# Kernel tuning notes

Hardware: AMD Instinct MI355X
Metric: run time of the kernel (lower is better)

Reference implementation:

```python
import jax, jax.numpy as jnp
import numpy as np

N_NODES = 50000
EPS = 1e-12  # F.normalize eps


def _gcn_layer(x, W, b, src, dst):
    # GCNConv(normalize=False): h = x @ W, then sum-aggregate messages from
    # source nodes into target nodes along edge_index, then add bias.
    h = x @ W
    agg = jax.ops.segment_sum(h[src], dst, num_segments=N_NODES)
    out = agg + b
    # F.normalize(p=2, dim=-1) then ReLU
    norm = jnp.linalg.norm(out, axis=-1, keepdims=True)
    out = out / jnp.maximum(norm, EPS)
    return jax.nn.relu(out)


def setup_inputs() -> dict:
    key = jax.random.key(0)
    ks = jax.random.split(key, 8)
    nfeat, nhid, nclass, n_edges = 128, 128, 40, 640000
    x = jax.random.normal(ks[0], (N_NODES, nfeat), dtype=jnp.float32)
    edge_index = jax.random.randint(ks[1], (2, n_edges), 0, N_NODES, dtype=jnp.int64)
    s = 1.0 / np.sqrt(nhid)
    return {
        "x": x,
        "edge_index": edge_index,
        "W1": jax.random.normal(ks[2], (nfeat, nhid), jnp.float32) * s,
        "b1": jnp.zeros((nhid,), jnp.float32),
        "W2": jax.random.normal(ks[3], (nhid, nhid), jnp.float32) * s,
        "b2": jnp.zeros((nhid,), jnp.float32),
        "W3": jax.random.normal(ks[4], (nhid, nhid), jnp.float32) * s,
        "b3": jnp.zeros((nhid,), jnp.float32),
        "W4": jax.random.normal(ks[5], (nhid, nhid), jnp.float32) * s,
        "b4": jnp.zeros((nhid,), jnp.float32),
        "Wl": jax.random.normal(ks[6], (nhid, nclass), jnp.float32) * s,
        "bl": jnp.zeros((nclass,), jnp.float32),
    }


def reference(x, edge_index, W1, b1, W2, b2, W3, b3, W4, b4, Wl, bl):
    src, dst = edge_index[0], edge_index[1]
    x1 = _gcn_layer(x, W1, b1, src, dst)
    x2 = _gcn_layer(x1, W2, b2, src, dst)
    x3 = _gcn_layer(x2, W3, b3, src, dst)
    x4 = _gcn_layer(x3, W4, b4, src, dst)
    logits = x4 @ Wl + bl
    probs = jax.nn.softmax(logits, axis=-1)
    return (logits, probs, x4)
```

## Files before the change

kernel.cpp:

```cpp
#include <hip/hip_runtime.h>
#include <hip/hip_bf16.h>
#include <hip/hip_fp16.h>
#include <math.h>

#define NFEAT 128
#define NCLASS 40

typedef __attribute__((ext_vector_type(8))) short frag_ab;
typedef __attribute__((ext_vector_type(4))) float frag_cd;

static __device__ inline unsigned short f2bf_rne(float f) {
    union { float f; unsigned u; } v;
    v.f = f;
    unsigned r = v.u + 0x7FFFu + ((v.u >> 16) & 1u);
    return (unsigned short)(r >> 16);
}
static __device__ inline float bf2f(unsigned short h) {
    union { unsigned u; float f; } v;
    v.u = ((unsigned)h) << 16;
    return v.f;
}


__global__ __launch_bounds__(256) void prep_kernel(const float* __restrict__ x,
                                                   __half* __restrict__ xh, int xc4,
                                                   int* __restrict__ cnt, int n_nodes,
                                                   const float* __restrict__ W0,
                                                   const float* __restrict__ W1,
                                                   const float* __restrict__ W2,
                                                   const float* __restrict__ W3,
                                                   short* __restrict__ whi,
                                                   short* __restrict__ wlo,
                                                   int convB, int zeroB) {
    int b = blockIdx.x;
    if (b < convB) {
        int i = b * 256 + threadIdx.x;
        if (i < xc4) {
            float4 v = ((const float4*)x)[i];
            ((__half2*)xh)[i * 2 + 0] = __floats2half2_rn(v.x, v.y);
            ((__half2*)xh)[i * 2 + 1] = __floats2half2_rn(v.z, v.w);
        }
    } else if (b < convB + zeroB) {
        int i = (b - convB) * 256 + threadIdx.x;
        if (i < n_nodes) cnt[i] = 0;
    } else {
        int wb = b - convB - zeroB;
        int layer = wb >> 3;
        const float* W = layer == 0 ? W0 : layer == 1 ? W1 : layer == 2 ? W2 : W3;
        short* h = whi + (size_t)layer * 16384;
        short* l = wlo + (size_t)layer * 16384;
        int idx = (wb & 7) * 256 + threadIdx.x;
        int lane = idx & 63;
        int t = (idx >> 6) & 7;
        int s = idx >> 9;
        int quad = lane >> 4;
        int n = lane & 15;
        int kbase = s * 32 + quad * 8;
        int col = t * 16 + n;
#pragma unroll
        for (int j = 0; j < 8; ++j) {
            float f = W[(size_t)(kbase + j) * NFEAT + col];
            unsigned short hb = f2bf_rne(f);
            unsigned short lb = f2bf_rne(f - bf2f(hb));
            h[(size_t)idx * 8 + j] = (short)hb;
            l[(size_t)idx * 8 + j] = (short)lb;
        }
    }
}


__global__ __launch_bounds__(256) void hist_kernel(const int* __restrict__ dst,
                                                   int* __restrict__ counts, int n_edges) {
    int i = blockIdx.x * 256 + threadIdx.x;
    int n4 = n_edges >> 2;
    if (i < n4) {
        int4 d = ((const int4*)dst)[i];
        atomicAdd(&counts[d.x], 1);
        atomicAdd(&counts[d.y], 1);
        atomicAdd(&counts[d.z], 1);
        atomicAdd(&counts[d.w], 1);
    }
    if (i == 0) {
        for (int e = n4 << 2; e < n_edges; ++e) atomicAdd(&counts[dst[e]], 1);
    }
}

__global__ __launch_bounds__(256) void scan1_kernel(const int* __restrict__ cnt,
                                                    int* __restrict__ excl,
                                                    int* __restrict__ bsums, int n) {
    __shared__ int sd[256];
    int t = threadIdx.x;
    int i = blockIdx.x * 256 + t;
    int v = (i < n) ? cnt[i] : 0;
    sd[t] = v;
    __syncthreads();
#pragma unroll
    for (int off = 1; off < 256; off <<= 1) {
        int tmp = (t >= off) ? sd[t - off] : 0;
        __syncthreads();
        sd[t] += tmp;
        __syncthreads();
    }
    if (i < n) excl[i] = sd[t] - v;
    if (t == 255) bsums[blockIdx.x] = sd[255];
}

__global__ __launch_bounds__(256) void scan2_kernel(int* __restrict__ bsums, int nb) {
    __shared__ int sd[256];
    int t = threadIdx.x;
    int v = (t < nb) ? bsums[t] : 0;
    sd[t] = v;
    __syncthreads();
#pragma unroll
    for (int off = 1; off < 256; off <<= 1) {
        int tmp = (t >= off) ? sd[t - off] : 0;
        __syncthreads();
        sd[t] += tmp;
        __syncthreads();
    }
    if (t < nb) bsums[t] = sd[t] - v;
    if (t == 255) bsums[nb] = sd[255];
}

__global__ __launch_bounds__(256) void scan3_kernel(const int* __restrict__ excl,
                                                    const int* __restrict__ bsums,
                                                    int* __restrict__ row_ptr,
                                                    int* __restrict__ woff, int n, int nb) {
    int i = blockIdx.x * 256 + threadIdx.x;
    if (i < n) {
        int v = excl[i] + bsums[blockIdx.x];
        row_ptr[i] = v;
        woff[i] = v;
    }
    if (i == 0) row_ptr[n] = bsums[nb];
}

__global__ __launch_bounds__(256) void scatter_kernel(const int* __restrict__ src,
                                                      const int* __restrict__ dst,
                                                      int* __restrict__ woff,
                                                      int* __restrict__ src_sorted, int n_edges) {
    int i = blockIdx.x * 256 + threadIdx.x;
    int n4 = n_edges >> 2;
    if (i < n4) {
        int4 d = ((const int4*)dst)[i];
        int4 s = ((const int4*)src)[i];
        int p0 = atomicAdd(&woff[d.x], 1);
        int p1 = atomicAdd(&woff[d.y], 1);
        int p2 = atomicAdd(&woff[d.z], 1);
        int p3 = atomicAdd(&woff[d.w], 1);
        src_sorted[p0] = s.x;
        src_sorted[p1] = s.y;
        src_sorted[p2] = s.z;
        src_sorted[p3] = s.w;
    }
    if (i == 0) {
        for (int e = n4 << 2; e < n_edges; ++e) {
            int p = atomicAdd(&woff[dst[e]], 1);
            src_sorted[p] = src[e];
        }
    }
}


__global__ __launch_bounds__(256) void agg_h_kernel(const __half* __restrict__ xin,
                                                    const int* __restrict__ row_ptr,
                                                    const int* __restrict__ src_sorted,
                                                    __half* __restrict__ aggh, int n_nodes) {
    int node = blockIdx.x * 16 + (threadIdx.x >> 4);
    if (node >= n_nodes) return;
    int c = threadIdx.x & 15;
    int jb = row_ptr[node], je = row_ptr[node + 1];
    const uint4* xp = (const uint4*)xin;

    float a[8];
#pragma unroll
    for (int i = 0; i < 8; ++i) a[i] = 0.f;

    int j = jb;
    for (; j + 3 < je; j += 4) {
        int s0 = src_sorted[j];
        int s1 = src_sorted[j + 1];
        int s2 = src_sorted[j + 2];
        int s3 = src_sorted[j + 3];
        uint4 r0 = xp[s0 * 16 + c];
        uint4 r1 = xp[s1 * 16 + c];
        uint4 r2 = xp[s2 * 16 + c];
        uint4 r3 = xp[s3 * 16 + c];
#pragma unroll
        for (int q = 0; q < 4; ++q) {
            unsigned u0 = (&r0.x)[q], u1 = (&r1.x)[q], u2 = (&r2.x)[q], u3 = (&r3.x)[q];
            float2 f0 = __half22float2(*(__half2*)&u0);
            float2 f1 = __half22float2(*(__half2*)&u1);
            float2 f2 = __half22float2(*(__half2*)&u2);
            float2 f3 = __half22float2(*(__half2*)&u3);
            a[q * 2 + 0] += f0.x + f1.x + f2.x + f3.x;
            a[q * 2 + 1] += f0.y + f1.y + f2.y + f3.y;
        }
    }
    for (; j < je; ++j) {
        int s0 = src_sorted[j];
        uint4 r0 = xp[s0 * 16 + c];
#pragma unroll
        for (int q = 0; q < 4; ++q) {
            unsigned u0 = (&r0.x)[q];
            float2 f0 = __half22float2(*(__half2*)&u0);
            a[q * 2 + 0] += f0.x;
            a[q * 2 + 1] += f0.y;
        }
    }
    __half2 h0 = __floats2half2_rn(a[0], a[1]);
    __half2 h1 = __floats2half2_rn(a[2], a[3]);
    __half2 h2 = __floats2half2_rn(a[4], a[5]);
    __half2 h3 = __floats2half2_rn(a[6], a[7]);
    uint4 o;
    o.x = *(unsigned*)&h0; o.y = *(unsigned*)&h1; o.z = *(unsigned*)&h2; o.w = *(unsigned*)&h3;
    ((uint4*)aggh)[(size_t)node * 16 + c] = o;
}


__global__ __launch_bounds__(256) void gemm_mfma_kernel(const __half* __restrict__ A,
                                                        const short* __restrict__ whi,
                                                        const short* __restrict__ wlo,
                                                        const float* __restrict__ bias,
                                                        float* __restrict__ outf,
                                                        __half* __restrict__ outh, int M) {
    int tid = threadIdx.x;
    int wave = tid >> 6;
    int lane = tid & 63;
    int quad = lane >> 4;
    int n16 = lane & 15;
    int base = blockIdx.x * 64;

    int arow = base + wave * 16 + n16;
    int arc = arow < M ? arow : M - 1;
    const __half* Ar = A + (size_t)arc * NFEAT;

    const frag_ab* WH = (const frag_ab*)whi;
    const frag_ab* WL = (const frag_ab*)wlo;

    frag_cd acc[8];
#pragma unroll
    for (int t = 0; t < 8; ++t) acc[t] = (frag_cd){0.f, 0.f, 0.f, 0.f};

#pragma unroll
    for (int s = 0; s < 4; ++s) {
        uint4 av = *(const uint4*)(Ar + s * 32 + quad * 8);
        frag_ab ah, al;
#pragma unroll
        for (int q = 0; q < 4; ++q) {
            unsigned u = (&av.x)[q];
            float2 f = __half22float2(*(__half2*)&u);
            unsigned short hb0 = f2bf_rne(f.x);
            unsigned short hb1 = f2bf_rne(f.y);
            ah[q * 2 + 0] = (short)hb0;
            ah[q * 2 + 1] = (short)hb1;
            al[q * 2 + 0] = (short)f2bf_rne(f.x - bf2f(hb0));
            al[q * 2 + 1] = (short)f2bf_rne(f.y - bf2f(hb1));
        }
#pragma unroll
        for (int t = 0; t < 8; ++t) {
            frag_ab bh = WH[(s * 8 + t) * 64 + lane];
            frag_ab bl = WL[(s * 8 + t) * 64 + lane];
            acc[t] = __builtin_amdgcn_mfma_f32_16x16x32_bf16(ah, bh, acc[t], 0, 0, 0);
            acc[t] = __builtin_amdgcn_mfma_f32_16x16x32_bf16(ah, bl, acc[t], 0, 0, 0);
            acc[t] = __builtin_amdgcn_mfma_f32_16x16x32_bf16(al, bh, acc[t], 0, 0, 0);
        }
    }

    float ssq[4] = {0.f, 0.f, 0.f, 0.f};
#pragma unroll
    for (int t = 0; t < 8; ++t) {
        float bv = bias[t * 16 + n16];
#pragma unroll
        for (int r = 0; r < 4; ++r) {
            acc[t][r] += bv;
            ssq[r] += acc[t][r] * acc[t][r];
        }
    }
#pragma unroll
    for (int mask = 1; mask <= 8; mask <<= 1) {
#pragma unroll
        for (int r = 0; r < 4; ++r) ssq[r] += __shfl_xor(ssq[r], mask);
    }
    float inv[4];
#pragma unroll
    for (int r = 0; r < 4; ++r) inv[r] = 1.0f / fmaxf(sqrtf(ssq[r]), 1e-12f);

    int orow0 = base + wave * 16 + quad * 4;
#pragma unroll
    for (int r = 0; r < 4; ++r) {
        int orow = orow0 + r;
        if (orow < M) {
            if (outh) {
                __half* op = outh + (size_t)orow * NFEAT + n16;
#pragma unroll
                for (int t = 0; t < 8; ++t)
                    op[t * 16] = __float2half(fmaxf(acc[t][r] * inv[r], 0.f));
            } else {
                float* op = outf + (size_t)orow * NFEAT + n16;
#pragma unroll
                for (int t = 0; t < 8; ++t)
                    op[t * 16] = fmaxf(acc[t][r] * inv[r], 0.f);
            }
        }
    }
}


__global__ __launch_bounds__(256) void classifier_kernel(const float* __restrict__ x4,
                                                         const float* __restrict__ Wl,
                                                         const float* __restrict__ bl,
                                                         float* __restrict__ logits,
                                                         float* __restrict__ probs, int n_nodes) {
    int node = blockIdx.x * 256 + threadIdx.x;
    int nc = node < n_nodes ? node : n_nodes - 1;
    const float* row = x4 + (size_t)nc * NFEAT;

    float acc[NCLASS];
#pragma unroll
    for (int c = 0; c < NCLASS; ++c) acc[c] = bl[c];

    for (int k = 0; k < NFEAT; k += 4) {
        float4 a = *(const float4*)(row + k);
#pragma unroll
        for (int kk = 0; kk < 4; ++kk) {
            float av = (&a.x)[kk];
            const float* Wr = Wl + (k + kk) * NCLASS;
#pragma unroll
            for (int c = 0; c < NCLASS; ++c) acc[c] += av * Wr[c];
        }
    }

    float m = acc[0];
#pragma unroll
    for (int c = 1; c < NCLASS; ++c) m = fmaxf(m, acc[c]);
    float ex[NCLASS];
    float sum = 0.f;
#pragma unroll
    for (int c = 0; c < NCLASS; ++c) {
        ex[c] = __expf(acc[c] - m);
        sum += ex[c];
    }
    float is = 1.0f / sum;

    if (node < n_nodes) {
        float4* lo = (float4*)(logits + (size_t)node * NCLASS);
        float4* po = (float4*)(probs + (size_t)node * NCLASS);
#pragma unroll
        for (int c = 0; c < NCLASS; c += 4) {
            float4 lv, pv;
            lv.x = acc[c + 0]; lv.y = acc[c + 1]; lv.z = acc[c + 2]; lv.w = acc[c + 3];
            pv.x = ex[c + 0] * is; pv.y = ex[c + 1] * is; pv.z = ex[c + 2] * is; pv.w = ex[c + 3] * is;
            lo[c >> 2] = lv;
            po[c >> 2] = pv;
        }
    }
}


extern "C" void kernel_launch(void* const* d_in, const int* in_sizes, int n_in,
                              void* d_out, int out_size, void* d_ws, size_t ws_size,
                              hipStream_t stream) {
    const float* x  = (const float*)d_in[0];
    const int*   ei = (const int*)d_in[1];
    const float* W1 = (const float*)d_in[2];
    const float* b1 = (const float*)d_in[3];
    const float* W2 = (const float*)d_in[4];
    const float* b2 = (const float*)d_in[5];
    const float* W3 = (const float*)d_in[6];
    const float* b3 = (const float*)d_in[7];
    const float* W4 = (const float*)d_in[8];
    const float* b4 = (const float*)d_in[9];
    const float* Wl = (const float*)d_in[10];
    const float* bl = (const float*)d_in[11];

    const int n_nodes = in_sizes[0] / NFEAT;
    const int n_edges = in_sizes[1] / 2;
    const int* src = ei;
    const int* dst = ei + n_edges;

    float* out    = (float*)d_out;
    float* logits = out;
    float* probs  = out + (size_t)n_nodes * NCLASS;
    float* x4     = out + 2 * (size_t)n_nodes * NCLASS;

    char* ws = (char*)d_ws;
    size_t off = 0;
    auto wsalloc = [&](size_t bytes) -> void* {
        void* p = ws + off;
        off += (bytes + 255) & ~(size_t)255;
        return p;
    };
    __half* aggh       = (__half*)wsalloc((size_t)n_nodes * NFEAT * sizeof(__half));
    __half* xh         = (__half*)wsalloc((size_t)n_nodes * NFEAT * sizeof(__half));
    int*    row_ptr    = (int*)wsalloc(((size_t)n_nodes + 1) * sizeof(int));
    int*    woff       = (int*)wsalloc((size_t)n_nodes * sizeof(int));
    int*    cnt        = (int*)wsalloc((size_t)n_nodes * sizeof(int));
    int*    src_sorted = (int*)wsalloc((size_t)n_edges * sizeof(int));
    int     nbt        = (n_nodes + 255) / 256;
    int*    bsums      = (int*)wsalloc(((size_t)nbt + 1) * sizeof(int));
    short*  whi        = (short*)wsalloc((size_t)4 * 16384 * sizeof(short));
    short*  wlo        = (short*)wsalloc((size_t)4 * 16384 * sizeof(short));

    int xc4   = (n_nodes * NFEAT) / 4;
    int convB = (xc4 + 255) / 256;
    int zeroB = (n_nodes + 255) / 256;
    prep_kernel<<<convB + zeroB + 32, 256, 0, stream>>>(x, xh, xc4, cnt, n_nodes,
                                                        W1, W2, W3, W4, whi, wlo,
                                                        convB, zeroB);

    int e4b = ((n_edges >> 2) + 255) / 256;
    hist_kernel<<<e4b, 256, 0, stream>>>(dst, cnt, n_edges);
    scan1_kernel<<<nbt, 256, 0, stream>>>(cnt, row_ptr , bsums, n_nodes);
    scan2_kernel<<<1, 256, 0, stream>>>(bsums, nbt);
    scan3_kernel<<<nbt, 256, 0, stream>>>(row_ptr, bsums, row_ptr, woff, n_nodes, nbt);
    scatter_kernel<<<e4b, 256, 0, stream>>>(src, dst, woff, src_sorted, n_edges);

    int ah = (n_nodes + 15) / 16;
    int gb = (n_nodes + 63) / 64;
    int cb = (n_nodes + 255) / 256;

    agg_h_kernel<<<ah, 256, 0, stream>>>(xh, row_ptr, src_sorted, aggh, n_nodes);
    gemm_mfma_kernel<<<gb, 256, 0, stream>>>(aggh, whi + 0 * 16384, wlo + 0 * 16384, b1, nullptr, xh, n_nodes);
    agg_h_kernel<<<ah, 256, 0, stream>>>(xh, row_ptr, src_sorted, aggh, n_nodes);
    gemm_mfma_kernel<<<gb, 256, 0, stream>>>(aggh, whi + 1 * 16384, wlo + 1 * 16384, b2, nullptr, xh, n_nodes);
    agg_h_kernel<<<ah, 256, 0, stream>>>(xh, row_ptr, src_sorted, aggh, n_nodes);
    gemm_mfma_kernel<<<gb, 256, 0, stream>>>(aggh, whi + 2 * 16384, wlo + 2 * 16384, b3, nullptr, xh, n_nodes);
    agg_h_kernel<<<ah, 256, 0, stream>>>(xh, row_ptr, src_sorted, aggh, n_nodes);
    gemm_mfma_kernel<<<gb, 256, 0, stream>>>(aggh, whi + 3 * 16384, wlo + 3 * 16384, b4, x4, nullptr, n_nodes);

    classifier_kernel<<<cb, 256, 0, stream>>>(x4, Wl, bl, logits, probs, n_nodes);
}
```

Measured before the change: 376.8 us.

## Fuse neighbor aggregation and MFMA GEMM into one kernel per GCN layer

Merges the gather-sum aggregation and the bf16-split MFMA GEMM into a single kernel. Each 64-node block aggregates into fp32 shared memory, then runs the GEMM from LDS. This removes the fp16 aggregate round-trip through global memory and four kernel launches, and keeps the aggregate in fp32 before the bf16 hi/lo split. The cost is about 33KB of LDS per block, which limits occupancy for the latency-bound gather phase, and ping-pong buffers are now needed because a layer can no longer overwrite its own input.

```diff
diff --git a/kernel.cpp b/kernel.cpp
--- a/kernel.cpp
+++ b/kernel.cpp
@@ -162,78 +162,75 @@
 }
 
 
-__global__ __launch_bounds__(256) void agg_h_kernel(const __half* __restrict__ xin,
-                                                    const int* __restrict__ row_ptr,
-                                                    const int* __restrict__ src_sorted,
-                                                    __half* __restrict__ aggh, int n_nodes) {
-    int node = blockIdx.x * 16 + (threadIdx.x >> 4);
-    if (node >= n_nodes) return;
-    int c = threadIdx.x & 15;
-    int jb = row_ptr[node], je = row_ptr[node + 1];
-    const uint4* xp = (const uint4*)xin;
-
-    float a[8];
-#pragma unroll
-    for (int i = 0; i < 8; ++i) a[i] = 0.f;
-
-    int j = jb;
-    for (; j + 3 < je; j += 4) {
-        int s0 = src_sorted[j];
-        int s1 = src_sorted[j + 1];
-        int s2 = src_sorted[j + 2];
-        int s3 = src_sorted[j + 3];
-        uint4 r0 = xp[s0 * 16 + c];
-        uint4 r1 = xp[s1 * 16 + c];
-        uint4 r2 = xp[s2 * 16 + c];
-        uint4 r3 = xp[s3 * 16 + c];
-#pragma unroll
-        for (int q = 0; q < 4; ++q) {
-            unsigned u0 = (&r0.x)[q], u1 = (&r1.x)[q], u2 = (&r2.x)[q], u3 = (&r3.x)[q];
-            float2 f0 = __half22float2(*(__half2*)&u0);
-            float2 f1 = __half22float2(*(__half2*)&u1);
-            float2 f2 = __half22float2(*(__half2*)&u2);
-            float2 f3 = __half22float2(*(__half2*)&u3);
-            a[q * 2 + 0] += f0.x + f1.x + f2.x + f3.x;
-            a[q * 2 + 1] += f0.y + f1.y + f2.y + f3.y;
-        }
-    }
-    for (; j < je; ++j) {
-        int s0 = src_sorted[j];
-        uint4 r0 = xp[s0 * 16 + c];
-#pragma unroll
-        for (int q = 0; q < 4; ++q) {
-            unsigned u0 = (&r0.x)[q];
-            float2 f0 = __half22float2(*(__half2*)&u0);
-            a[q * 2 + 0] += f0.x;
-            a[q * 2 + 1] += f0.y;
-        }
-    }
-    __half2 h0 = __floats2half2_rn(a[0], a[1]);
-    __half2 h1 = __floats2half2_rn(a[2], a[3]);
-    __half2 h2 = __floats2half2_rn(a[4], a[5]);
-    __half2 h3 = __floats2half2_rn(a[6], a[7]);
-    uint4 o;
-    o.x = *(unsigned*)&h0; o.y = *(unsigned*)&h1; o.z = *(unsigned*)&h2; o.w = *(unsigned*)&h3;
-    ((uint4*)aggh)[(size_t)node * 16 + c] = o;
-}
-
-
-__global__ __launch_bounds__(256) void gemm_mfma_kernel(const __half* __restrict__ A,
+__global__ __launch_bounds__(256) void gcn_fused_kernel(const __half* __restrict__ xin,
+                                                        const int* __restrict__ row_ptr,
+                                                        const int* __restrict__ src_sorted,
                                                         const short* __restrict__ whi,
                                                         const short* __restrict__ wlo,
                                                         const float* __restrict__ bias,
                                                         float* __restrict__ outf,
                                                         __half* __restrict__ outh, int M) {
+    __shared__ float smem[64][132];
     int tid = threadIdx.x;
+    int base = blockIdx.x * 64;
+
+    {
+        int c = tid & 15;
+        int sub = tid >> 4;
+        const uint4* xp = (const uint4*)xin;
+#pragma unroll 1
+        for (int p = 0; p < 4; ++p) {
+            int nl = p * 16 + sub;
+            int node = base + nl;
+            float a[8];
+#pragma unroll
+            for (int i = 0; i < 8; ++i) a[i] = 0.f;
+            int jb = 0, je = 0;
+            if (node < M) { jb = row_ptr[node]; je = row_ptr[node + 1]; }
+            int j = jb;
+            for (; j + 3 < je; j += 4) {
+                int s0 = src_sorted[j];
+                int s1 = src_sorted[j + 1];
+                int s2 = src_sorted[j + 2];
+                int s3 = src_sorted[j + 3];
+                uint4 r0 = xp[s0 * 16 + c];
+                uint4 r1 = xp[s1 * 16 + c];
+                uint4 r2 = xp[s2 * 16 + c];
+                uint4 r3 = xp[s3 * 16 + c];
+#pragma unroll
+                for (int q = 0; q < 4; ++q) {
+                    unsigned u0 = (&r0.x)[q], u1 = (&r1.x)[q], u2 = (&r2.x)[q], u3 = (&r3.x)[q];
+                    float2 f0 = __half22float2(*(__half2*)&u0);
+                    float2 f1 = __half22float2(*(__half2*)&u1);
+                    float2 f2 = __half22float2(*(__half2*)&u2);
+                    float2 f3 = __half22float2(*(__half2*)&u3);
+                    a[q * 2 + 0] += f0.x + f1.x + f2.x + f3.x;
+                    a[q * 2 + 1] += f0.y + f1.y + f2.y + f3.y;
+                }
+            }
+            for (; j < je; ++j) {
+                int s0 = src_sorted[j];
+                uint4 r0 = xp[s0 * 16 + c];
+#pragma unroll
+                for (int q = 0; q < 4; ++q) {
+                    unsigned u0 = (&r0.x)[q];
+                    float2 f0 = __half22float2(*(__half2*)&u0);
+                    a[q * 2 + 0] += f0.x;
+                    a[q * 2 + 1] += f0.y;
+                }
+            }
+            float4* wp = (float4*)&smem[nl][c * 8];
+            wp[0] = make_float4(a[0], a[1], a[2], a[3]);
+            wp[1] = make_float4(a[4], a[5], a[6], a[7]);
+        }
+    }
+    __syncthreads();
+
     int wave = tid >> 6;
     int lane = tid & 63;
     int quad = lane >> 4;
     int n16 = lane & 15;
-    int base = blockIdx.x * 64;
-
-    int arow = base + wave * 16 + n16;
-    int arc = arow < M ? arow : M - 1;
-    const __half* Ar = A + (size_t)arc * NFEAT;
+    int lrow = wave * 16 + n16;
 
     const frag_ab* WH = (const frag_ab*)whi;
     const frag_ab* WL = (const frag_ab*)wlo;
@@ -244,18 +241,16 @@
 
 #pragma unroll
     for (int s = 0; s < 4; ++s) {
-        uint4 av = *(const uint4*)(Ar + s * 32 + quad * 8);
+        const float* ap = &smem[lrow][s * 32 + quad * 8];
+        float4 v0 = *(const float4*)(ap);
+        float4 v1 = *(const float4*)(ap + 4);
+        float fv[8] = {v0.x, v0.y, v0.z, v0.w, v1.x, v1.y, v1.z, v1.w};
         frag_ab ah, al;
 #pragma unroll
-        for (int q = 0; q < 4; ++q) {
-            unsigned u = (&av.x)[q];
-            float2 f = __half22float2(*(__half2*)&u);
-            unsigned short hb0 = f2bf_rne(f.x);
-            unsigned short hb1 = f2bf_rne(f.y);
-            ah[q * 2 + 0] = (short)hb0;
-            ah[q * 2 + 1] = (short)hb1;
-            al[q * 2 + 0] = (short)f2bf_rne(f.x - bf2f(hb0));
-            al[q * 2 + 1] = (short)f2bf_rne(f.y - bf2f(hb1));
+        for (int jj = 0; jj < 8; ++jj) {
+            unsigned short hb = f2bf_rne(fv[jj]);
+            ah[jj] = (short)hb;
+            al[jj] = (short)f2bf_rne(fv[jj] - bf2f(hb));
         }
 #pragma unroll
         for (int t = 0; t < 8; ++t) {
@@ -391,8 +386,8 @@
         off += (bytes + 255) & ~(size_t)255;
         return p;
     };
-    __half* aggh       = (__half*)wsalloc((size_t)n_nodes * NFEAT * sizeof(__half));
     __half* xh         = (__half*)wsalloc((size_t)n_nodes * NFEAT * sizeof(__half));
+    __half* xh2        = (__half*)wsalloc((size_t)n_nodes * NFEAT * sizeof(__half));
     int*    row_ptr    = (int*)wsalloc(((size_t)n_nodes + 1) * sizeof(int));
     int*    woff       = (int*)wsalloc((size_t)n_nodes * sizeof(int));
     int*    cnt        = (int*)wsalloc((size_t)n_nodes * sizeof(int));
@@ -416,18 +411,13 @@
     scan3_kernel<<<nbt, 256, 0, stream>>>(row_ptr, bsums, row_ptr, woff, n_nodes, nbt);
     scatter_kernel<<<e4b, 256, 0, stream>>>(src, dst, woff, src_sorted, n_edges);
 
-    int ah = (n_nodes + 15) / 16;
     int gb = (n_nodes + 63) / 64;
     int cb = (n_nodes + 255) / 256;
 
-    agg_h_kernel<<<ah, 256, 0, stream>>>(xh, row_ptr, src_sorted, aggh, n_nodes);
-    gemm_mfma_kernel<<<gb, 256, 0, stream>>>(aggh, whi + 0 * 16384, wlo + 0 * 16384, b1, nullptr, xh, n_nodes);
-    agg_h_kernel<<<ah, 256, 0, stream>>>(xh, row_ptr, src_sorted, aggh, n_nodes);
-    gemm_mfma_kernel<<<gb, 256, 0, stream>>>(aggh, whi + 1 * 16384, wlo + 1 * 16384, b2, nullptr, xh, n_nodes);
-    agg_h_kernel<<<ah, 256, 0, stream>>>(xh, row_ptr, src_sorted, aggh, n_nodes);
-    gemm_mfma_kernel<<<gb, 256, 0, stream>>>(aggh, whi + 2 * 16384, wlo + 2 * 16384, b3, nullptr, xh, n_nodes);
-    agg_h_kernel<<<ah, 256, 0, stream>>>(xh, row_ptr, src_sorted, aggh, n_nodes);
-    gemm_mfma_kernel<<<gb, 256, 0, stream>>>(aggh, whi + 3 * 16384, wlo + 3 * 16384, b4, x4, nullptr, n_nodes);
+    gcn_fused_kernel<<<gb, 256, 0, stream>>>(xh,  row_ptr, src_sorted, whi + 0 * 16384, wlo + 0 * 16384, b1, nullptr, xh2, n_nodes);
+    gcn_fused_kernel<<<gb, 256, 0, stream>>>(xh2, row_ptr, src_sorted, whi + 1 * 16384, wlo + 1 * 16384, b2, nullptr, xh,  n_nodes);
+    gcn_fused_kernel<<<gb, 256, 0, stream>>>(xh,  row_ptr, src_sorted, whi + 2 * 16384, wlo + 2 * 16384, b3, nullptr, xh2, n_nodes);
+    gcn_fused_kernel<<<gb, 256, 0, stream>>>(xh2, row_ptr, src_sorted, whi + 3 * 16384, wlo + 3 * 16384, b4, x4, nullptr, n_nodes);
 
     classifier_kernel<<<cb, 256, 0, stream>>>(x4, Wl, bl, logits, probs, n_nodes);
 }
```

New measurement: 349.4 us. 1.08x faster.
